# Kernel optimization log

Hardware: AMD Instinct MI355X
Metric: run time of the kernel (lower is better)

The kernel has to match this reference:

```python
import jax, jax.numpy as jnp
import numpy as np

IN_F, OUT_F = 4096, 11008
IN_G, OUT_G = 8, 1
NUM_CB, CB_SIZE = 2, 256


def setup_inputs() -> dict:
    key = jax.random.key(0)
    k1, k2, k3, k4, k5 = jax.random.split(key, 5)
    no, ni = OUT_F // OUT_G, IN_F // IN_G
    x = jax.random.normal(k1, (4, 2048, IN_F), dtype=jnp.float32)
    codes = jax.random.randint(k2, (no, ni, NUM_CB), 0, CB_SIZE, dtype=jnp.int32)
    codebooks = jax.random.normal(k3, (NUM_CB, CB_SIZE, OUT_G, IN_G), dtype=jnp.float32)
    scales = jax.random.uniform(k4, (no, 1, 1, 1), dtype=jnp.float32) + 0.5
    bias = jax.random.normal(k5, (OUT_F,), dtype=jnp.float32)
    return {"x": x, "codes": codes, "codebooks": codebooks, "scales": scales, "bias": bias}


def _dequantize_weight(codes, codebooks, scales):
    # codes: [no, ni, M] ints; codebooks: [M, C, og, ig]; scales: [no, 1, 1, 1]
    M = codebooks.shape[0]
    og, ig = codebooks.shape[2], codebooks.shape[3]
    no, ni = codes.shape[0], codes.shape[1]
    # gather each codebook's entry and sum over codebooks -> [no, ni, og, ig]
    m_idx = jnp.arange(M)[None, None, :]
    gathered = codebooks[m_idx, codes]            # [no, ni, M, og, ig]
    deq = gathered.sum(axis=2) * scales           # [no, ni, og, ig]
    # reorder groups back to dense weight [out_features, in_features]
    return deq.transpose(0, 2, 1, 3).reshape(no * og, ni * ig)


def reference(x, codes, codebooks, scales, bias):
    w = _dequantize_weight(codes, codebooks, scales)  # [OUT_F, IN_F]
    return jnp.einsum("bsi,oi->bso", x, w) + bias
```

## Files before the change

kernel.cpp:

```cpp
#include <hip/hip_runtime.h>
#include <hip/hip_bf16.h>
#include <stdint.h>

#define IN_F   4096
#define OUT_F  11008
#define M_TOK  8192

typedef __attribute__((ext_vector_type(4))) int   int32x4;

__device__ __forceinline__ float block_rowmax(float m, float* red, int t) {
    red[t] = m; __syncthreads();
    for (int s = 128; s > 0; s >>= 1) {
        if (t < s) red[t] = fmaxf(red[t], red[t + s]);
        __syncthreads();
    }
    float r = red[0]; __syncthreads();
    return fmaxf(r, 1e-8f);
}

__global__ __launch_bounds__(256) void k_qx(
        const float* __restrict__ x, signed char* __restrict__ Xq,
        float* __restrict__ sx) {
    __shared__ float red[256];
    int r = blockIdx.x, t = threadIdx.x;
    const float4* xr = (const float4*)(x + (size_t)r * IN_F) + t * 4;
    float4 v0 = xr[0], v1 = xr[1], v2 = xr[2], v3 = xr[3];
    float m = 0.f;
#define MX4(v) m = fmaxf(m, fmaxf(fmaxf(fabsf(v.x), fabsf(v.y)), fmaxf(fabsf(v.z), fabsf(v.w))))
    MX4(v0); MX4(v1); MX4(v2); MX4(v3);
    float rm = block_rowmax(m, red, t);
    if (t == 0) sx[r] = rm / 127.f;
    float inv = 127.f / rm;
    union { signed char c[16]; uint4 u; } pk;
#define Q4(v, o) pk.c[o] = (signed char)__float2int_rn(v.x * inv);            \
                 pk.c[o+1] = (signed char)__float2int_rn(v.y * inv);          \
                 pk.c[o+2] = (signed char)__float2int_rn(v.z * inv);          \
                 pk.c[o+3] = (signed char)__float2int_rn(v.w * inv)
    Q4(v0, 0); Q4(v1, 4); Q4(v2, 8); Q4(v3, 12);
    *(uint4*)(Xq + (size_t)r * IN_F + t * 16) = pk.u;
}

__global__ __launch_bounds__(256) void k_qw(
        const int* __restrict__ codes,
        const float* __restrict__ codebooks,
        const float* __restrict__ scales,
        signed char* __restrict__ Wq, float* __restrict__ sw) {
    __shared__ float cb[4096];
    __shared__ float red[256];
    int o = blockIdx.x, t = threadIdx.x;
    {
        const float4* cbg = (const float4*)codebooks;
        float4* cbl = (float4*)cb;
#pragma unroll
        for (int i = 0; i < 4; ++i) cbl[t + i * 256] = cbg[t + i * 256];
    }
    __syncthreads();
    const int2* cp = (const int2*)codes + (size_t)o * 512 + t * 2;
    int2 c0 = cp[0], c1 = cp[1];
    float e[16]; float m = 0.f;
#pragma unroll
    for (int j = 0; j < 8; ++j) {
        e[j]     = cb[c0.x * 8 + j] + cb[2048 + c0.y * 8 + j];
        e[8 + j] = cb[c1.x * 8 + j] + cb[2048 + c1.y * 8 + j];
    }
#pragma unroll
    for (int j = 0; j < 16; ++j) m = fmaxf(m, fabsf(e[j]));
    float rm = block_rowmax(m, red, t);
    if (t == 0) sw[o] = scales[o] * rm / 127.f;
    float inv = 127.f / rm;
    union { signed char c[16]; uint4 u; } pk;
#pragma unroll
    for (int j = 0; j < 16; ++j) pk.c[j] = (signed char)__float2int_rn(e[j] * inv);
    *(uint4*)(Wq + (size_t)o * IN_F + t * 16) = pk.u;
}


#define BARRIER() __builtin_amdgcn_s_barrier()
#define VMW(n)    asm volatile("s_waitcnt vmcnt(" #n ")")

#define GL16(gp, lp) __builtin_amdgcn_global_load_lds(                        \
    (const __attribute__((address_space(1))) void*)(gp),                      \
    (__attribute__((address_space(3))) void*)(lp), 16, 0, 0)

__global__ __launch_bounds__(512, 2) void k_gemm(
        const signed char* __restrict__ A,
        const signed char* __restrict__ B,
        const float* __restrict__ sx,
        const float* __restrict__ sw,
        const float* __restrict__ bias,
        float* __restrict__ out) {
    __shared__ signed char lA0[256 * 128];
    __shared__ signed char lA1[256 * 128];
    __shared__ signed char lB0[256 * 128];
    __shared__ signed char lB1[256 * 128];

    const int tid = threadIdx.x;
    const int l = tid & 63;
    const int w = tid >> 6;
    const int wm = w >> 2, wn = w & 3;

    int lid = blockIdx.x;
    int xcd = lid & 7, j = lid >> 3;
    int bx = j >> 2;
    int by = (xcd << 2) + (j & 3);
    const int rowBase = by * 256;
    const int colBase = bx * 256;

    const int srow = w * 8 + (l >> 3);
    const int scol = ((l & 7) ^ ((l >> 3) & 7)) << 4;
    const signed char* gA = A + (size_t)(rowBase + srow) * IN_F + scol;
    const signed char* gB = B + (size_t)(colBase + srow) * IN_F + scol;
    signed char* lA0w = &lA0[w * 8 * 128];
    signed char* lA1w = &lA1[w * 8 * 128];
    signed char* lB0w = &lB0[w * 8 * 128];
    signed char* lB1w = &lB1[w * 8 * 128];

#define STAGEH_(P, t, H) do {                                                 \
    const signed char* _g = ((H) ? gB : gA) + (size_t)(t) * 128;              \
    signed char* _l = ((H) ? lB##P##w : lA##P##w);                            \
    GL16(_g,                       _l);                                       \
    GL16(_g +  64 * IN_F,          _l +  64 * 128);                           \
    GL16(_g + 128 * IN_F,          _l + 128 * 128);                           \
    GL16(_g + 192 * IN_F,          _l + 192 * 128);                           \
} while (0)

    const int frow = l & 15, g = l >> 4;
    const int cho0 = ((g ^ (frow & 7)) << 4);
    const int cho1 = (((4 + g) ^ (frow & 7)) << 4);
    const char* rowA0 = (const char*)&lA0[(wm * 128 + frow) * 128];
    const char* rowA1 = (const char*)&lA1[(wm * 128 + frow) * 128];
    const char* rowB0 = (const char*)&lB0[(wn * 64 + frow) * 128];
    const char* rowB1 = (const char*)&lB1[(wn * 64 + frow) * 128];
#define LDA_(P, m, kk) (*(const int32x4*)(rowA##P + (m) * 2048 + ((kk) ? cho1 : cho0)))
#define LDB_(P, n, kk) (*(const int32x4*)(rowB##P + (n) * 2048 + ((kk) ? cho1 : cho0)))

    int32x4 acc[8][4] = {};
    int32x4 ar[4][2];
    int32x4 brA[2][2];
    int32x4 brB[2][2];

#define QUADQ(M0, N0, BR) do {                                                \
    __builtin_amdgcn_s_setprio(1);                                            \
    _Pragma("unroll") for (int mm = 0; mm < 4; ++mm)                          \
    _Pragma("unroll") for (int nn = 0; nn < 2; ++nn)                          \
    _Pragma("unroll") for (int kk = 0; kk < 2; ++kk)                          \
        acc[(M0) + mm][(N0) + nn] = __builtin_amdgcn_mfma_i32_16x16x64_i8(    \
            ar[mm][kk], BR[nn][kk], acc[(M0) + mm][(N0) + nn], 0, 0, 0);      \
    __builtin_amdgcn_s_setprio(0);                                            \
} while (0)

#define RD_AR03(P) do {                                                       \
    _Pragma("unroll") for (int mm = 0; mm < 4; ++mm) {                        \
        ar[mm][0] = LDA_(P, mm, 0); ar[mm][1] = LDA_(P, mm, 1); }             \
} while (0)
#define RD_AR47(P) do {                                                       \
    _Pragma("unroll") for (int mm = 0; mm < 4; ++mm) {                        \
        ar[mm][0] = LDA_(P, 4 + mm, 0); ar[mm][1] = LDA_(P, 4 + mm, 1); }     \
} while (0)
#define RD_BR01(P) do {                                                       \
    brA[0][0] = LDB_(P, 0, 0); brA[0][1] = LDB_(P, 0, 1);                     \
    brA[1][0] = LDB_(P, 1, 0); brA[1][1] = LDB_(P, 1, 1);                     \
} while (0)
#define RD_BR23(P) do {                                                       \
    brB[0][0] = LDB_(P, 2, 0); brB[0][1] = LDB_(P, 2, 1);                     \
    brB[1][0] = LDB_(P, 3, 0); brB[1][1] = LDB_(P, 3, 1);                     \
} while (0)

    STAGEH_(0, 0, 0); STAGEH_(0, 0, 1);
    STAGEH_(1, 1, 1);
    VMW(4); BARRIER();
    RD_AR03(0); RD_BR01(0);
    STAGEH_(1, 1, 0);
    BARRIER();

    for (int i = 0; i < 15; ++i) {
        int t = 2 * i;
        QUADQ(0, 0, brA);
        RD_BR23(0);
        BARRIER();
        QUADQ(0, 2, brB);
        RD_AR47(0);
        BARRIER();
        QUADQ(4, 2, brB);
        STAGEH_(0, t + 2, 1);
        VMW(4); BARRIER();
        QUADQ(4, 0, brA);
        RD_AR03(1); RD_BR01(1);
        STAGEH_(0, t + 2, 0);
        BARRIER();
        QUADQ(0, 0, brA);
        RD_BR23(1);
        BARRIER();
        QUADQ(0, 2, brB);
        RD_AR47(1);
        BARRIER();
        QUADQ(4, 2, brB);
        STAGEH_(1, t + 3, 1);
        VMW(4); BARRIER();
        QUADQ(4, 0, brA);
        RD_AR03(0); RD_BR01(0);
        STAGEH_(1, t + 3, 0);
        BARRIER();
    }

    QUADQ(0, 0, brA);
    RD_BR23(0);
    BARRIER();
    QUADQ(0, 2, brB);
    RD_AR47(0);
    BARRIER();
    QUADQ(4, 2, brB);
    VMW(0); BARRIER();
    QUADQ(4, 0, brA);
    RD_AR03(1); RD_BR01(1);
    BARRIER();
    QUADQ(0, 0, brA);
    RD_BR23(1);
    BARRIER();
    QUADQ(0, 2, brB);
    RD_AR47(1);
    BARRIER();
    QUADQ(4, 2, brB);
    QUADQ(4, 0, brA);

#pragma unroll
    for (int n = 0; n < 4; ++n) {
        int gcol = colBase + wn * 64 + n * 16 + frow;
        float swv = sw[gcol];
        float bv = bias[gcol];
#pragma unroll
        for (int m = 0; m < 8; ++m) {
            int grow0 = rowBase + wm * 128 + m * 16 + g * 4;
            float4 sx4 = *(const float4*)&sx[grow0];
            out[(size_t)(grow0 + 0) * OUT_F + gcol] = (float)acc[m][n][0] * sx4.x * swv + bv;
            out[(size_t)(grow0 + 1) * OUT_F + gcol] = (float)acc[m][n][1] * sx4.y * swv + bv;
            out[(size_t)(grow0 + 2) * OUT_F + gcol] = (float)acc[m][n][2] * sx4.z * swv + bv;
            out[(size_t)(grow0 + 3) * OUT_F + gcol] = (float)acc[m][n][3] * sx4.w * swv + bv;
        }
    }
}

extern "C" void kernel_launch(void* const* d_in, const int* in_sizes, int n_in,
                              void* d_out, int out_size, void* d_ws, size_t ws_size,
                              hipStream_t stream) {
    const float* x         = (const float*)d_in[0];
    const int*   codes     = (const int*)d_in[1];
    const float* codebooks = (const float*)d_in[2];
    const float* scales    = (const float*)d_in[3];
    const float* bias      = (const float*)d_in[4];
    float* out = (float*)d_out;

    signed char* Wq = (signed char*)d_ws;
    signed char* Xq = Wq + (size_t)OUT_F * IN_F;
    float* sx = (float*)(Xq + (size_t)M_TOK * IN_F);
    float* sw = sx + M_TOK;

    k_qx<<<M_TOK, 256, 0, stream>>>(x, Xq, sx);
    k_qw<<<OUT_F, 256, 0, stream>>>(codes, codebooks, scales, Wq, sw);
    k_gemm<<<1376, 512, 0, stream>>>(Xq, Wq, sx, sw, bias, out);
}
```

Baseline: 469.6 us.

## Merge quantize kernels into one launch and pin MFMA/LDS interleave with sched barriers

Merges the activation and weight quantization kernels into a single k_prep launch, with the block index choosing which path runs. This removes one launch and lets the two prep workloads overlap. In the int8 GEMM main loop, the s_setprio calls around the MFMA groups are dropped. Sched_group_barrier pins are added instead so MFMAs interleave with LDS reads and global-to-LDS loads in a fixed pattern. The goal is better overlap of memory ops with matrix work, at the risk of constraining the compiler's scheduler or giving worse interleaving than it would choose itself.

```diff
diff --git a/kernel.cpp b/kernel.cpp
--- a/kernel.cpp
+++ b/kernel.cpp
@@ -8,75 +8,88 @@
 
 typedef __attribute__((ext_vector_type(4))) int   int32x4;
 
-__device__ __forceinline__ float block_rowmax(float m, float* red, int t) {
-    red[t] = m; __syncthreads();
-    for (int s = 128; s > 0; s >>= 1) {
-        if (t < s) red[t] = fmaxf(red[t], red[t + s]);
-        __syncthreads();
-    }
-    float r = red[0]; __syncthreads();
-    return fmaxf(r, 1e-8f);
-}
-
-__global__ __launch_bounds__(256) void k_qx(
-        const float* __restrict__ x, signed char* __restrict__ Xq,
-        float* __restrict__ sx) {
+__global__ __launch_bounds__(256) void k_prep(
+        const float* __restrict__ x,
+        const int* __restrict__ codes,
+        const float* __restrict__ codebooks,
+        const float* __restrict__ scales,
+        signed char* __restrict__ Xq, float* __restrict__ sx,
+        signed char* __restrict__ Wq, float* __restrict__ sw) {
+    __shared__ float cb[4096];
     __shared__ float red[256];
-    int r = blockIdx.x, t = threadIdx.x;
-    const float4* xr = (const float4*)(x + (size_t)r * IN_F) + t * 4;
-    float4 v0 = xr[0], v1 = xr[1], v2 = xr[2], v3 = xr[3];
-    float m = 0.f;
+    int t = threadIdx.x;
+
+    if (blockIdx.x < M_TOK) {
+        int r = blockIdx.x;
+        const float4* xr = (const float4*)(x + (size_t)r * IN_F) + t * 4;
+        float4 v0 = xr[0], v1 = xr[1], v2 = xr[2], v3 = xr[3];
+        float m = 0.f;
 #define MX4(v) m = fmaxf(m, fmaxf(fmaxf(fabsf(v.x), fabsf(v.y)), fmaxf(fabsf(v.z), fabsf(v.w))))
-    MX4(v0); MX4(v1); MX4(v2); MX4(v3);
-    float rm = block_rowmax(m, red, t);
-    if (t == 0) sx[r] = rm / 127.f;
-    float inv = 127.f / rm;
-    union { signed char c[16]; uint4 u; } pk;
+        MX4(v0); MX4(v1); MX4(v2); MX4(v3);
+        red[t] = m; __syncthreads();
+        for (int s = 128; s > 0; s >>= 1) {
+            if (t < s) red[t] = fmaxf(red[t], red[t + s]);
+            __syncthreads();
+        }
+        float rm = fmaxf(red[0], 1e-8f);
+        if (t == 0) sx[r] = rm / 127.f;
+        float inv = 127.f / rm;
+        union { signed char c[16]; uint4 u; } pk;
 #define Q4(v, o) pk.c[o] = (signed char)__float2int_rn(v.x * inv);            \
                  pk.c[o+1] = (signed char)__float2int_rn(v.y * inv);          \
                  pk.c[o+2] = (signed char)__float2int_rn(v.z * inv);          \
                  pk.c[o+3] = (signed char)__float2int_rn(v.w * inv)
-    Q4(v0, 0); Q4(v1, 4); Q4(v2, 8); Q4(v3, 12);
-    *(uint4*)(Xq + (size_t)r * IN_F + t * 16) = pk.u;
-}
-
-__global__ __launch_bounds__(256) void k_qw(
-        const int* __restrict__ codes,
-        const float* __restrict__ codebooks,
-        const float* __restrict__ scales,
-        signed char* __restrict__ Wq, float* __restrict__ sw) {
-    __shared__ float cb[4096];
-    __shared__ float red[256];
-    int o = blockIdx.x, t = threadIdx.x;
-    {
-        const float4* cbg = (const float4*)codebooks;
-        float4* cbl = (float4*)cb;
-#pragma unroll
-        for (int i = 0; i < 4; ++i) cbl[t + i * 256] = cbg[t + i * 256];
+        Q4(v0, 0); Q4(v1, 4); Q4(v2, 8); Q4(v3, 12);
+        *(uint4*)(Xq + (size_t)r * IN_F + t * 16) = pk.u;
+    } else {
+        int o = blockIdx.x - M_TOK;
+        {
+            const float4* cbg = (const float4*)codebooks;
+            float4* cbl = (float4*)cb;
+#pragma unroll
+            for (int i = 0; i < 4; ++i) cbl[t + i * 256] = cbg[t + i * 256];
+        }
+        __syncthreads();
+        const int2* cp = (const int2*)codes + (size_t)o * 512 + t * 2;
+        int2 c0 = cp[0], c1 = cp[1];
+        float e[16]; float m = 0.f;
+#pragma unroll
+        for (int j = 0; j < 8; ++j) {
+            e[j]     = cb[c0.x * 8 + j] + cb[2048 + c0.y * 8 + j];
+            e[8 + j] = cb[c1.x * 8 + j] + cb[2048 + c1.y * 8 + j];
+        }
+#pragma unroll
+        for (int j = 0; j < 16; ++j) m = fmaxf(m, fabsf(e[j]));
+        red[t] = m; __syncthreads();
+        for (int s = 128; s > 0; s >>= 1) {
+            if (t < s) red[t] = fmaxf(red[t], red[t + s]);
+            __syncthreads();
+        }
+        float rm = fmaxf(red[0], 1e-8f);
+        if (t == 0) sw[o] = scales[o] * rm / 127.f;
+        float inv = 127.f / rm;
+        union { signed char c[16]; uint4 u; } pk;
+#pragma unroll
+        for (int j = 0; j < 16; ++j) pk.c[j] = (signed char)__float2int_rn(e[j] * inv);
+        *(uint4*)(Wq + (size_t)o * IN_F + t * 16) = pk.u;
     }
-    __syncthreads();
-    const int2* cp = (const int2*)codes + (size_t)o * 512 + t * 2;
-    int2 c0 = cp[0], c1 = cp[1];
-    float e[16]; float m = 0.f;
-#pragma unroll
-    for (int j = 0; j < 8; ++j) {
-        e[j]     = cb[c0.x * 8 + j] + cb[2048 + c0.y * 8 + j];
-        e[8 + j] = cb[c1.x * 8 + j] + cb[2048 + c1.y * 8 + j];
-    }
-#pragma unroll
-    for (int j = 0; j < 16; ++j) m = fmaxf(m, fabsf(e[j]));
-    float rm = block_rowmax(m, red, t);
-    if (t == 0) sw[o] = scales[o] * rm / 127.f;
-    float inv = 127.f / rm;
-    union { signed char c[16]; uint4 u; } pk;
-#pragma unroll
-    for (int j = 0; j < 16; ++j) pk.c[j] = (signed char)__float2int_rn(e[j] * inv);
-    *(uint4*)(Wq + (size_t)o * IN_F + t * 16) = pk.u;
 }
 
 
 #define BARRIER() __builtin_amdgcn_s_barrier()
 #define VMW(n)    asm volatile("s_waitcnt vmcnt(" #n ")")
+#define SGB(mask, n) __builtin_amdgcn_sched_group_barrier(mask, n, 0)
+
+#define PIN_M16_D4()  do { SGB(8,4); SGB(0x100,1); SGB(8,4); SGB(0x100,1);   \
+                           SGB(8,4); SGB(0x100,1); SGB(8,4); SGB(0x100,1); } while (0)
+#define PIN_M16_D8()  do { SGB(8,4); SGB(0x100,2); SGB(8,4); SGB(0x100,2);   \
+                           SGB(8,4); SGB(0x100,2); SGB(8,4); SGB(0x100,2); } while (0)
+#define PIN_M16_V4()  do { SGB(8,4); SGB(0x10,1);  SGB(8,4); SGB(0x10,1);    \
+                           SGB(8,4); SGB(0x10,1);  SGB(8,4); SGB(0x10,1); } while (0)
+#define PIN_M16_D12_V4() do { SGB(8,4); SGB(0x100,3); SGB(0x10,1);           \
+                              SGB(8,4); SGB(0x100,3); SGB(0x10,1);           \
+                              SGB(8,4); SGB(0x100,3); SGB(0x10,1);           \
+                              SGB(8,4); SGB(0x100,3); SGB(0x10,1); } while (0)
 
 #define GL16(gp, lp) __builtin_amdgcn_global_load_lds(                        \
     (const __attribute__((address_space(1))) void*)(gp),                      \
@@ -140,13 +153,11 @@
     int32x4 brB[2][2];
 
 #define QUADQ(M0, N0, BR) do {                                                \
-    __builtin_amdgcn_s_setprio(1);                                            \
     _Pragma("unroll") for (int mm = 0; mm < 4; ++mm)                          \
     _Pragma("unroll") for (int nn = 0; nn < 2; ++nn)                          \
     _Pragma("unroll") for (int kk = 0; kk < 2; ++kk)                          \
         acc[(M0) + mm][(N0) + nn] = __builtin_amdgcn_mfma_i32_16x16x64_i8(    \
             ar[mm][kk], BR[nn][kk], acc[(M0) + mm][(N0) + nn], 0, 0, 0);      \
-    __builtin_amdgcn_s_setprio(0);                                            \
 } while (0)
 
 #define RD_AR03(P) do {                                                       \
@@ -177,29 +188,37 @@
         int t = 2 * i;
         QUADQ(0, 0, brA);
         RD_BR23(0);
+        PIN_M16_D4();
         BARRIER();
         QUADQ(0, 2, brB);
         RD_AR47(0);
+        PIN_M16_D8();
         BARRIER();
         QUADQ(4, 2, brB);
         STAGEH_(0, t + 2, 1);
+        PIN_M16_V4();
         VMW(4); BARRIER();
         QUADQ(4, 0, brA);
         RD_AR03(1); RD_BR01(1);
         STAGEH_(0, t + 2, 0);
+        PIN_M16_D12_V4();
         BARRIER();
         QUADQ(0, 0, brA);
         RD_BR23(1);
+        PIN_M16_D4();
         BARRIER();
         QUADQ(0, 2, brB);
         RD_AR47(1);
+        PIN_M16_D8();
         BARRIER();
         QUADQ(4, 2, brB);
         STAGEH_(1, t + 3, 1);
+        PIN_M16_V4();
         VMW(4); BARRIER();
         QUADQ(4, 0, brA);
         RD_AR03(0); RD_BR01(0);
         STAGEH_(1, t + 3, 0);
+        PIN_M16_D12_V4();
         BARRIER();
     }
 
@@ -255,7 +274,7 @@
     float* sx = (float*)(Xq + (size_t)M_TOK * IN_F);
     float* sw = sx + M_TOK;
 
-    k_qx<<<M_TOK, 256, 0, stream>>>(x, Xq, sx);
-    k_qw<<<OUT_F, 256, 0, stream>>>(codes, codebooks, scales, Wq, sw);
+    k_prep<<<M_TOK + OUT_F, 256, 0, stream>>>(x, codes, codebooks, scales,
+                                              Xq, sx, Wq, sw);
     k_gemm<<<1376, 512, 0, stream>>>(Xq, Wq, sx, sw, bias, out);
 }
```

Measured after the change: 464.7 us. No clear change (-1.0%).
